# Optimization experiments

Hardware: AMD Instinct MI355X
Metric: run time of the kernel (lower is better)

Reference implementation:

```python
import jax, jax.numpy as jnp
import numpy as np

IMG_SIZE = np.array([960.0, 512.0], np.float32)   # network input size (w, h)
HM_SIZE = np.array([480.0, 256.0], np.float32)    # heatmap size = IMG_SIZE / 2 (w, h)
GRID_SIZE = np.array([8000.0, 8000.0, 2000.0], np.float32)  # mm
CUBE = (80, 80, 20)
NBINS = CUBE[0] * CUBE[1] * CUBE[2]


def _base_grid():
    # linspace(-size/2, size/2, nbins) per axis, meshgrid indexing='ij' (torch default)
    axes = [np.linspace(-GRID_SIZE[d] / 2, GRID_SIZE[d] / 2, CUBE[d], dtype=np.float32) for d in range(3)]
    gx, gy, gz = np.meshgrid(*axes, indexing='ij')
    return jnp.asarray(np.stack([gx.ravel(), gy.ravel(), gz.ravel()], axis=1))  # [NBINS, 3]


def _bilinear_sample(img, coords):
    # img: [C,H,W]; coords: [P,2] normalized to [-1,1], align_corners=True, zero padding
    C, H, W = img.shape
    ix = (coords[:, 0] + 1.0) * 0.5 * (W - 1)
    iy = (coords[:, 1] + 1.0) * 0.5 * (H - 1)
    x0 = jnp.floor(ix)
    y0 = jnp.floor(iy)
    x1 = x0 + 1.0
    y1 = y0 + 1.0
    wx1 = ix - x0
    wx0 = 1.0 - wx1
    wy1 = iy - y0
    wy0 = 1.0 - wy1

    def corner(xi, yi, w):
        valid = (xi >= 0) & (xi <= W - 1) & (yi >= 0) & (yi <= H - 1)
        xc = jnp.clip(xi, 0, W - 1).astype(jnp.int32)
        yc = jnp.clip(yi, 0, H - 1).astype(jnp.int32)
        vals = img[:, yc, xc]  # [C,P]
        return vals * (w * valid.astype(img.dtype))[None, :]

    return (corner(x0, y0, wx0 * wy0) + corner(x1, y0, wx1 * wy0)
            + corner(x0, y1, wx0 * wy1) + corner(x1, y1, wx1 * wy1))  # [C,P]


def reference(heatmaps, R, T, f, c_cam, trans, wh, grid_center):
    # heatmaps: [N,B,C,H,W]; R:[N,B,3,3]; T:[N,B,3]; f,c_cam,wh:[N,B,2]; trans:[N,B,2,3]; grid_center:[B,3]
    N, B, C, H, W = heatmaps.shape
    hm = jnp.asarray(HM_SIZE)
    img_sz = jnp.asarray(IMG_SIZE)

    grids = _base_grid()[None, :, :] + grid_center[:, None, :]          # [B,P,3]
    pts = grids[None, :, :, :] - T[:, :, None, :]                        # [N,B,P,3]
    xcam = jnp.einsum('nbij,nbpj->nbpi', R, pts)                         # [N,B,P,3]
    xy = f[:, :, None, :] * (xcam[..., :2] / xcam[..., 2:3]) + c_cam[:, :, None, :]  # pixel coords

    bnd = jnp.all((xy >= 0) & (xy < wh[:, :, None, :]), axis=-1).astype(heatmaps.dtype)  # [N,B,P]

    mx = jnp.max(wh, axis=-1)[:, :, None, None]
    xy = jnp.minimum(jnp.maximum(xy, -1.0), mx)
    xy1 = jnp.concatenate([xy, jnp.ones_like(xy[..., :1])], axis=-1)     # homogeneous
    xy = jnp.einsum('nbij,nbpj->nbpi', trans, xy1)                       # affine to network image space
    xy = xy * (hm / img_sz)
    sg = jnp.clip(xy / (hm - 1.0) * 2.0 - 1.0, -1.1, 1.1)                # [N,B,P,2]

    samples = jax.vmap(_bilinear_sample)(
        heatmaps.reshape(N * B, C, H, W), sg.reshape(N * B, NBINS, 2)
    ).reshape(N, B, C, NBINS)                                            # [N,B,C,P]

    bnd_e = bnd[:, :, None, :]                                           # [N,B,1,P]
    cubes = jnp.sum(samples * bnd_e, axis=0) / (jnp.sum(bnd_e, axis=0) + 1e-6)  # [B,C,P]
    cubes = jnp.nan_to_num(cubes)
    cubes = jnp.clip(cubes, 0.0, 1.0)  # feature_op = False
    cubes = cubes.reshape(B, C, CUBE[0], CUBE[1], CUBE[2])
    return cubes, grids


def setup_inputs():
    key = jax.random.key(0)
    k_hm, k_gc = jax.random.split(key)
    N, B, C, H, W = 5, 8, 15, 256, 480
    heatmaps = jax.random.uniform(k_hm, (N, B, C, H, W), jnp.float32)

    # plausible look-at cameras around the space center
    center = np.array([0.0, -500.0, 800.0], np.float32)
    Rs, Ts = [], []
    for i in range(N):
        ang = 2.0 * np.pi * i / N
        pos = center + np.array([6000.0 * np.cos(ang), 6000.0 * np.sin(ang), 1200.0], np.float32)
        fwd = center - pos
        fwd = fwd / np.linalg.norm(fwd)
        up = np.array([0.0, 0.0, 1.0], np.float32)
        right = np.cross(fwd, up)
        right = right / np.linalg.norm(right)
        down = np.cross(fwd, right)
        Rs.append(np.stack([right, down, fwd]).astype(np.float32))
        Ts.append(pos)
    R = jnp.asarray(np.broadcast_to(np.stack(Rs)[:, None], (N, B, 3, 3)).copy())
    T = jnp.asarray(np.broadcast_to(np.stack(Ts)[:, None], (N, B, 3)).copy())
    f = jnp.full((N, B, 2), 1500.0, jnp.float32)
    wh_np = np.array([1920.0, 1080.0], np.float32)  # original image width/height
    c_cam = jnp.asarray(np.broadcast_to(wh_np / 2, (N, B, 2)).copy())
    s = IMG_SIZE / wh_np
    tr = np.array([[s[0], 0.0, 0.0], [0.0, s[1], 0.0]], np.float32)
    trans = jnp.asarray(np.broadcast_to(tr, (N, B, 2, 3)).copy())
    wh = jnp.asarray(np.broadcast_to(wh_np, (N, B, 2)).copy())
    grid_center = jnp.asarray(center)[None, :] + 200.0 * jax.random.normal(k_gc, (B, 3), jnp.float32)
    return dict(heatmaps=heatmaps, R=R, T=T, f=f, c_cam=c_cam, trans=trans, wh=wh, grid_center=grid_center)
```

## Files before the change

kernel.cpp:

```cpp
#include <hip/hip_runtime.h>
#include <stdint.h>

#define N_VIEWS 5
#define B_ 8
#define C_ 15
#define CP_ 16
#define H_ 256
#define W_ 480
#define NBINS 128000
#define HW_ (H_ * W_)
#define CUBES_ELEMS (B_ * C_ * NBINS)
#define NB_ (N_VIEWS * B_)

typedef float v2f __attribute__((ext_vector_type(2)));

__global__ __launch_bounds__(256) void transpose_fp8_kernel(
    const float* __restrict__ hm, uint32_t* __restrict__ tp)
{
    const int idx = blockIdx.x * 256 + threadIdx.x;
    const int cb  = blockIdx.y;
    if (idx >= HW_) return;
    const float* src = hm + (size_t)cb * C_ * HW_ + idx;
    float v[CP_];
#pragma unroll
    for (int c = 0; c < C_; ++c) v[c] = src[(size_t)c * HW_];
    v[15] = 0.0f;
    uint32_t w[4];
#pragma unroll
    for (int j = 0; j < 4; ++j) {
        int r = 0;
        r = __builtin_amdgcn_cvt_pk_fp8_f32(v[4*j + 0], v[4*j + 1], r, false);
        r = __builtin_amdgcn_cvt_pk_fp8_f32(v[4*j + 2], v[4*j + 3], r, true);
        w[j] = (uint32_t)r;
    }
    uint4* dst = (uint4*)(tp + ((size_t)cb * HW_ + (size_t)idx) * 4);
    *dst = make_uint4(w[0], w[1], w[2], w[3]);
}

struct Corner4 { int o00, o10, o01, o11; float w00, w10, w01, w11; bool inb; };

__device__ __forceinline__ Corner4 project_one(
    int cb, float gx, float gy, float gz,
    const float* __restrict__ R, const float* __restrict__ T,
    const float* __restrict__ f, const float* __restrict__ ccam,
    const float* __restrict__ trans, const float* __restrict__ wh)
{
    Corner4 r; r.inb = false;
    const float* Rn = R + cb * 9;
    const float px = gx - T[cb * 3 + 0];
    const float py = gy - T[cb * 3 + 1];
    const float pz = gz - T[cb * 3 + 2];
    const float xcm = Rn[0] * px + Rn[1] * py + Rn[2] * pz;
    const float ycm = Rn[3] * px + Rn[4] * py + Rn[5] * pz;
    const float zcm = Rn[6] * px + Rn[7] * py + Rn[8] * pz;
    const float u = f[cb * 2 + 0] * (xcm / zcm) + ccam[cb * 2 + 0];
    const float v = f[cb * 2 + 1] * (ycm / zcm) + ccam[cb * 2 + 1];
    const float w0 = wh[cb * 2 + 0], w1 = wh[cb * 2 + 1];
    if (!((u >= 0.0f) && (u < w0) && (v >= 0.0f) && (v < w1))) return r;
    r.inb = true;
    const float mx = fmaxf(w0, w1);
    const float uu = fminf(fmaxf(u, -1.0f), mx);
    const float vv = fminf(fmaxf(v, -1.0f), mx);
    const float* tr = trans + cb * 6;
    const float tx = (tr[0] * uu + tr[1] * vv + tr[2]) * 0.5f;
    const float ty = (tr[3] * uu + tr[4] * vv + tr[5]) * 0.5f;
    const float sgx = fminf(fmaxf(tx / 479.0f * 2.0f - 1.0f, -1.1f), 1.1f);
    const float sgy = fminf(fmaxf(ty / 255.0f * 2.0f - 1.0f, -1.1f), 1.1f);
    const float ixf = (sgx + 1.0f) * 0.5f * 479.0f;
    const float iyf = (sgy + 1.0f) * 0.5f * 255.0f;
    const float x0 = floorf(ixf), y0 = floorf(iyf);
    const float x1 = x0 + 1.0f, y1 = y0 + 1.0f;
    const float wx1 = ixf - x0, wy1 = iyf - y0;
    const float wx0 = 1.0f - wx1, wy0 = 1.0f - wy1;
    const float v00 = (x0 >= 0.0f && y0 >= 0.0f) ? 1.0f : 0.0f;
    const float v10 = (x1 <= 479.0f && y0 >= 0.0f) ? 1.0f : 0.0f;
    const float v01 = (x0 >= 0.0f && y1 <= 255.0f) ? 1.0f : 0.0f;
    const float v11 = (x1 <= 479.0f && y1 <= 255.0f) ? 1.0f : 0.0f;
    r.w00 = wx0 * wy0 * v00; r.w10 = wx1 * wy0 * v10;
    r.w01 = wx0 * wy1 * v01; r.w11 = wx1 * wy1 * v11;
    const int xi0 = min(max((int)x0, 0), W_ - 1);
    const int yi0 = min(max((int)y0, 0), H_ - 1);
    const int xi1 = min(max((int)x1, 0), W_ - 1);
    const int yi1 = min(max((int)y1, 0), H_ - 1);
    r.o00 = yi0 * W_ + xi0; r.o10 = yi0 * W_ + xi1;
    r.o01 = yi1 * W_ + xi0; r.o11 = yi1 * W_ + xi1;
    return r;
}

__device__ __forceinline__ void decode_grid(int p, int b, const float* __restrict__ gc,
                                            float& gx, float& gy, float& gz)
{
    const int ixg = p / 1600;
    const int rem = p - ixg * 1600;
    const int iyg = rem / 20;
    const int izg = rem - iyg * 20;
    gx = (float)(-4000.0 + ixg * (8000.0 / 79.0)) + gc[b * 3 + 0];
    gy = (float)(-4000.0 + iyg * (8000.0 / 79.0)) + gc[b * 3 + 1];
    gz = (float)(-1000.0 + izg * (2000.0 / 19.0)) + gc[b * 3 + 2];
}

__device__ __forceinline__ void acc_pixel(float* acc, uint4 q, float wgt)
{
    if (wgt == 0.0f) return;
    const uint32_t u[4] = { q.x, q.y, q.z, q.w };
#pragma unroll
    for (int j = 0; j < 4; ++j) {
        v2f lo = __builtin_amdgcn_cvt_pk_f32_fp8(u[j], false);
        v2f hi = __builtin_amdgcn_cvt_pk_f32_fp8(u[j], true);
        acc[4*j + 0] += wgt * lo.x;
        acc[4*j + 1] += wgt * lo.y;
        acc[4*j + 2] += wgt * hi.x;
        acc[4*j + 3] += wgt * hi.y;
    }
}

__global__ __launch_bounds__(256) void project_kernel_fp8(
    const uint32_t* __restrict__ tp,
    const float* __restrict__ R, const float* __restrict__ T,
    const float* __restrict__ f, const float* __restrict__ ccam,
    const float* __restrict__ trans, const float* __restrict__ wh,
    const float* __restrict__ gc,
    float* __restrict__ out)
{
    const int p = blockIdx.x * blockDim.x + threadIdx.x;
    const int b = blockIdx.y;
    if (p >= NBINS) return;

    float gx, gy, gz;
    decode_grid(p, b, gc, gx, gy, gz);
    {
        const size_t goff = (size_t)CUBES_ELEMS + ((size_t)b * NBINS + (size_t)p) * 3;
        out[goff + 0] = gx; out[goff + 1] = gy; out[goff + 2] = gz;
    }

    float acc[CP_];
#pragma unroll
    for (int c = 0; c < CP_; ++c) acc[c] = 0.0f;
    float bndsum = 0.0f;

#pragma unroll
    for (int n = 0; n < N_VIEWS; ++n) {
        const int cb = n * B_ + b;
        Corner4 cr = project_one(cb, gx, gy, gz, R, T, f, ccam, trans, wh);
        if (cr.inb) {
            bndsum += 1.0f;
            const uint4* base = (const uint4*)tp + (size_t)cb * HW_;
            const uint4 q00 = base[cr.o00];
            const uint4 q10 = base[cr.o10];
            const uint4 q01 = base[cr.o01];
            const uint4 q11 = base[cr.o11];
            acc_pixel(acc, q00, cr.w00);
            acc_pixel(acc, q10, cr.w10);
            acc_pixel(acc, q01, cr.w01);
            acc_pixel(acc, q11, cr.w11);
        }
    }

    const float inv = 1.0f / (bndsum + 1e-6f);
    const size_t ob = (size_t)b * C_ * NBINS + (size_t)p;
#pragma unroll
    for (int c = 0; c < C_; ++c) {
        float r = acc[c] * inv;
        r = fmaxf(r, 0.0f);
        r = fminf(r, 1.0f);
        out[ob + (size_t)c * NBINS] = r;
    }
}

__global__ __launch_bounds__(256) void project_kernel_direct(
    const float* __restrict__ hm,
    const float* __restrict__ R, const float* __restrict__ T,
    const float* __restrict__ f, const float* __restrict__ ccam,
    const float* __restrict__ trans, const float* __restrict__ wh,
    const float* __restrict__ gc,
    float* __restrict__ out)
{
    const int p = blockIdx.x * blockDim.x + threadIdx.x;
    const int b = blockIdx.y;
    if (p >= NBINS) return;
    float gx, gy, gz;
    decode_grid(p, b, gc, gx, gy, gz);
    {
        const size_t goff = (size_t)CUBES_ELEMS + ((size_t)b * NBINS + (size_t)p) * 3;
        out[goff + 0] = gx; out[goff + 1] = gy; out[goff + 2] = gz;
    }
    float acc[C_];
#pragma unroll
    for (int c = 0; c < C_; ++c) acc[c] = 0.0f;
    float bndsum = 0.0f;
#pragma unroll
    for (int n = 0; n < N_VIEWS; ++n) {
        const int cb = n * B_ + b;
        Corner4 cr = project_one(cb, gx, gy, gz, R, T, f, ccam, trans, wh);
        if (cr.inb) {
            bndsum += 1.0f;
            const float* img = hm + (size_t)cb * C_ * HW_;
#pragma unroll
            for (int c = 0; c < C_; ++c) {
                const float* ic = img + (size_t)c * HW_;
                acc[c] += cr.w00 * ic[cr.o00] + cr.w10 * ic[cr.o10]
                        + cr.w01 * ic[cr.o01] + cr.w11 * ic[cr.o11];
            }
        }
    }
    const float inv = 1.0f / (bndsum + 1e-6f);
    const size_t ob = (size_t)b * C_ * NBINS + (size_t)p;
#pragma unroll
    for (int c = 0; c < C_; ++c) {
        float r = acc[c] * inv;
        r = fmaxf(r, 0.0f);
        r = fminf(r, 1.0f);
        out[ob + (size_t)c * NBINS] = r;
    }
}

extern "C" void kernel_launch(void* const* d_in, const int* in_sizes, int n_in,
                              void* d_out, int out_size, void* d_ws, size_t ws_size,
                              hipStream_t stream) {
    const float* hm    = (const float*)d_in[0];
    const float* R     = (const float*)d_in[1];
    const float* T     = (const float*)d_in[2];
    const float* f     = (const float*)d_in[3];
    const float* ccam  = (const float*)d_in[4];
    const float* trans = (const float*)d_in[5];
    const float* wh    = (const float*)d_in[6];
    const float* gc    = (const float*)d_in[7];
    float* out = (float*)d_out;

    const size_t ws_needed = (size_t)NB_ * HW_ * CP_;

    if (ws_size >= ws_needed) {
        uint32_t* tp = (uint32_t*)d_ws;
        dim3 tgrid((HW_ + 255) / 256, NB_);
        transpose_fp8_kernel<<<tgrid, 256, 0, stream>>>(hm, tp);
        dim3 grid(NBINS / 256, B_);
        project_kernel_fp8<<<grid, 256, 0, stream>>>(tp, R, T, f, ccam, trans, wh, gc, out);
    } else {
        dim3 grid(NBINS / 256, B_);
        project_kernel_direct<<<grid, 256, 0, stream>>>(hm, R, T, f, ccam, trans, wh, gc, out);
    }
}
```

Baseline: 504.4 us.

## Make projection branchless and issue all view gathers before accumulating

The projection now computes a validity mask instead of returning early. Out-of-bounds views gather from offset 0 with zero weights. All 20 corner gathers across the five views are issued up front, so memory latency overlaps instead of being serialized behind per-view branches. The launch grid is also flattened so that consecutive blocks interleave the batch index, which may improve cache locality across batches. The cost is higher register pressure (20 uint4 held live) and loads for views that would otherwise be skipped.

```diff
diff --git a/kernel.cpp b/kernel.cpp
--- a/kernel.cpp
+++ b/kernel.cpp
@@ -37,15 +37,15 @@
     *dst = make_uint4(w[0], w[1], w[2], w[3]);
 }
 
-struct Corner4 { int o00, o10, o01, o11; float w00, w10, w01, w11; bool inb; };
-
-__device__ __forceinline__ Corner4 project_one(
+struct Proj { int o00, o10, o01, o11; float w00, w10, w01, w11, inb; };
+
+__device__ __forceinline__ Proj project_one(
     int cb, float gx, float gy, float gz,
     const float* __restrict__ R, const float* __restrict__ T,
     const float* __restrict__ f, const float* __restrict__ ccam,
     const float* __restrict__ trans, const float* __restrict__ wh)
 {
-    Corner4 r; r.inb = false;
+    Proj r;
     const float* Rn = R + cb * 9;
     const float px = gx - T[cb * 3 + 0];
     const float py = gy - T[cb * 3 + 1];
@@ -56,8 +56,8 @@
     const float u = f[cb * 2 + 0] * (xcm / zcm) + ccam[cb * 2 + 0];
     const float v = f[cb * 2 + 1] * (ycm / zcm) + ccam[cb * 2 + 1];
     const float w0 = wh[cb * 2 + 0], w1 = wh[cb * 2 + 1];
-    if (!((u >= 0.0f) && (u < w0) && (v >= 0.0f) && (v < w1))) return r;
-    r.inb = true;
+    const bool inb = (u >= 0.0f) & (u < w0) & (v >= 0.0f) & (v < w1);
+    const float inbf = inb ? 1.0f : 0.0f;
     const float mx = fmaxf(w0, w1);
     const float uu = fminf(fmaxf(u, -1.0f), mx);
     const float vv = fminf(fmaxf(v, -1.0f), mx);
@@ -72,18 +72,21 @@
     const float x1 = x0 + 1.0f, y1 = y0 + 1.0f;
     const float wx1 = ixf - x0, wy1 = iyf - y0;
     const float wx0 = 1.0f - wx1, wy0 = 1.0f - wy1;
-    const float v00 = (x0 >= 0.0f && y0 >= 0.0f) ? 1.0f : 0.0f;
-    const float v10 = (x1 <= 479.0f && y0 >= 0.0f) ? 1.0f : 0.0f;
-    const float v01 = (x0 >= 0.0f && y1 <= 255.0f) ? 1.0f : 0.0f;
-    const float v11 = (x1 <= 479.0f && y1 <= 255.0f) ? 1.0f : 0.0f;
+    const float v00 = (x0 >= 0.0f && y0 >= 0.0f) ? inbf : 0.0f;
+    const float v10 = (x1 <= 479.0f && y0 >= 0.0f) ? inbf : 0.0f;
+    const float v01 = (x0 >= 0.0f && y1 <= 255.0f) ? inbf : 0.0f;
+    const float v11 = (x1 <= 479.0f && y1 <= 255.0f) ? inbf : 0.0f;
     r.w00 = wx0 * wy0 * v00; r.w10 = wx1 * wy0 * v10;
     r.w01 = wx0 * wy1 * v01; r.w11 = wx1 * wy1 * v11;
     const int xi0 = min(max((int)x0, 0), W_ - 1);
     const int yi0 = min(max((int)y0, 0), H_ - 1);
     const int xi1 = min(max((int)x1, 0), W_ - 1);
     const int yi1 = min(max((int)y1, 0), H_ - 1);
-    r.o00 = yi0 * W_ + xi0; r.o10 = yi0 * W_ + xi1;
-    r.o01 = yi1 * W_ + xi0; r.o11 = yi1 * W_ + xi1;
+    const int o00 = yi0 * W_ + xi0, o10 = yi0 * W_ + xi1;
+    const int o01 = yi1 * W_ + xi0, o11 = yi1 * W_ + xi1;
+    r.o00 = inb ? o00 : 0; r.o10 = inb ? o10 : 0;
+    r.o01 = inb ? o01 : 0; r.o11 = inb ? o11 : 0;
+    r.inb = inbf;
     return r;
 }
 
@@ -101,7 +104,6 @@
 
 __device__ __forceinline__ void acc_pixel(float* acc, uint4 q, float wgt)
 {
-    if (wgt == 0.0f) return;
     const uint32_t u[4] = { q.x, q.y, q.z, q.w };
 #pragma unroll
     for (int j = 0; j < 4; ++j) {
@@ -122,8 +124,9 @@
     const float* __restrict__ gc,
     float* __restrict__ out)
 {
-    const int p = blockIdx.x * blockDim.x + threadIdx.x;
-    const int b = blockIdx.y;
+    const int bid = blockIdx.x;
+    const int b   = bid & 7;
+    const int p   = (bid >> 3) * 256 + (int)threadIdx.x;
     if (p >= NBINS) return;
 
     float gx, gy, gz;
@@ -133,27 +136,30 @@
         out[goff + 0] = gx; out[goff + 1] = gy; out[goff + 2] = gz;
     }
 
+    Proj pr[N_VIEWS];
+    uint4 q[N_VIEWS][4];
+#pragma unroll
+    for (int n = 0; n < N_VIEWS; ++n) {
+        const int cb = n * B_ + b;
+        pr[n] = project_one(cb, gx, gy, gz, R, T, f, ccam, trans, wh);
+        const uint4* base = (const uint4*)tp + (size_t)cb * HW_;
+        q[n][0] = base[pr[n].o00];
+        q[n][1] = base[pr[n].o10];
+        q[n][2] = base[pr[n].o01];
+        q[n][3] = base[pr[n].o11];
+    }
+
     float acc[CP_];
 #pragma unroll
     for (int c = 0; c < CP_; ++c) acc[c] = 0.0f;
     float bndsum = 0.0f;
-
 #pragma unroll
     for (int n = 0; n < N_VIEWS; ++n) {
-        const int cb = n * B_ + b;
-        Corner4 cr = project_one(cb, gx, gy, gz, R, T, f, ccam, trans, wh);
-        if (cr.inb) {
-            bndsum += 1.0f;
-            const uint4* base = (const uint4*)tp + (size_t)cb * HW_;
-            const uint4 q00 = base[cr.o00];
-            const uint4 q10 = base[cr.o10];
-            const uint4 q01 = base[cr.o01];
-            const uint4 q11 = base[cr.o11];
-            acc_pixel(acc, q00, cr.w00);
-            acc_pixel(acc, q10, cr.w10);
-            acc_pixel(acc, q01, cr.w01);
-            acc_pixel(acc, q11, cr.w11);
-        }
+        bndsum += pr[n].inb;
+        acc_pixel(acc, q[n][0], pr[n].w00);
+        acc_pixel(acc, q[n][1], pr[n].w10);
+        acc_pixel(acc, q[n][2], pr[n].w01);
+        acc_pixel(acc, q[n][3], pr[n].w11);
     }
 
     const float inv = 1.0f / (bndsum + 1e-6f);
@@ -191,16 +197,14 @@
 #pragma unroll
     for (int n = 0; n < N_VIEWS; ++n) {
         const int cb = n * B_ + b;
-        Corner4 cr = project_one(cb, gx, gy, gz, R, T, f, ccam, trans, wh);
-        if (cr.inb) {
-            bndsum += 1.0f;
-            const float* img = hm + (size_t)cb * C_ * HW_;
-#pragma unroll
-            for (int c = 0; c < C_; ++c) {
-                const float* ic = img + (size_t)c * HW_;
-                acc[c] += cr.w00 * ic[cr.o00] + cr.w10 * ic[cr.o10]
-                        + cr.w01 * ic[cr.o01] + cr.w11 * ic[cr.o11];
-            }
+        Proj cr = project_one(cb, gx, gy, gz, R, T, f, ccam, trans, wh);
+        bndsum += cr.inb;
+        const float* img = hm + (size_t)cb * C_ * HW_;
+#pragma unroll
+        for (int c = 0; c < C_; ++c) {
+            const float* ic = img + (size_t)c * HW_;
+            acc[c] += cr.w00 * ic[cr.o00] + cr.w10 * ic[cr.o10]
+                    + cr.w01 * ic[cr.o01] + cr.w11 * ic[cr.o11];
         }
     }
     const float inv = 1.0f / (bndsum + 1e-6f);
@@ -233,7 +237,7 @@
         uint32_t* tp = (uint32_t*)d_ws;
         dim3 tgrid((HW_ + 255) / 256, NB_);
         transpose_fp8_kernel<<<tgrid, 256, 0, stream>>>(hm, tp);
-        dim3 grid(NBINS / 256, B_);
+        dim3 grid((NBINS / 256) * B_);
         project_kernel_fp8<<<grid, 256, 0, stream>>>(tp, R, T, f, ccam, trans, wh, gc, out);
     } else {
         dim3 grid(NBINS / 256, B_);
```

Result: faster. 481.0 us (-4.7%).
